# Optimization experiments

Measured on AMD Instinct MI355X. Metric: run time of the kernel, lower is better.

Reference implementation:

```python
import jax, jax.numpy as jnp
import numpy as np

N, E, G = 100000, 400000, 2000   # nodes, edges, graphs
IN, H = 48, 128                  # in_channels, hidden_channels (= out_channels)
L = 6                            # num GIN layers
EPS = 1e-5                       # BatchNorm eps
SLOPE = 0.01                     # leaky_relu negative slope


def setup_inputs() -> dict:
    key = jax.random.key(0)
    ks = jax.random.split(key, 12)
    x = jax.random.normal(ks[0], (N, IN), jnp.float32)
    edge_index = jax.random.randint(ks[1], (2, E), 0, N)
    edge_attr = jax.random.normal(ks[2], (E, 4), jnp.float32)  # ignored by GINConv
    # sorted graph-assignment vector; guarantee every graph has >=1 node
    batch = jnp.sort(jnp.concatenate([jnp.arange(G),
                                      jax.random.randint(ks[3], (N - G,), 0, G)]))
    s = 0.05
    W1a = jax.random.normal(ks[4], (IN, H), jnp.float32) * s        # layer-0 MLP lin1
    W1b = jax.random.normal(ks[5], (L - 1, H, H), jnp.float32) * s  # layers 1..5 MLP lin1
    b1 = jnp.zeros((L, H), jnp.float32)
    g1 = jnp.ones((L, H), jnp.float32)    # inner BN scale
    be1 = jnp.zeros((L, H), jnp.float32)  # inner BN bias
    W2 = jax.random.normal(ks[6], (L, H, H), jnp.float32) * s       # MLP lin2
    b2 = jnp.zeros((L, H), jnp.float32)
    gn = jnp.ones((L - 1, H), jnp.float32)    # outer BN scale (layers 0..4)
    bn_b = jnp.zeros((L - 1, H), jnp.float32) # outer BN bias
    fc_w = jax.random.normal(ks[7], (2 * H, 64), jnp.float32) * s
    fc_b = jnp.zeros((64,), jnp.float32)
    fc2_w = jax.random.normal(ks[8], (64, 3), jnp.float32) * s
    fc2_b = jnp.zeros((3,), jnp.float32)
    return dict(x=x, edge_attr=edge_attr, W1a=W1a, W1b=W1b, b1=b1, g1=g1, be1=be1,
                W2=W2, b2=b2, gn=gn, bn_b=bn_b, fc_w=fc_w, fc_b=fc_b,
                fc2_w=fc2_w, fc2_b=fc2_b, edge_index=edge_index, batch=batch,
                num_graphs=G)


def _bn(h, g, b):
    # training-mode BatchNorm1d over node dim (biased variance, as torch)
    m = jnp.mean(h, axis=0)
    v = jnp.mean((h - m) ** 2, axis=0)
    return g * (h - m) * jax.lax.rsqrt(v + EPS) + b


def _lrelu(h):
    return jnp.where(h >= 0, h, SLOPE * h)


def reference(x, edge_attr, W1a, W1b, b1, g1, be1, W2, b2, gn, bn_b,
              fc_w, fc_b, fc2_w, fc2_b, edge_index, batch, num_graphs):
    del edge_attr  # GINConv does not use edge attributes
    src, dst = edge_index[0], edge_index[1]
    n = x.shape[0]
    h = x
    for l in range(L):
        # GINConv: (1 + eps) * x + sum_{j in N(i)} x_j, eps = 0
        agg = jax.ops.segment_sum(h[src], dst, num_segments=n)
        z = h + agg
        W1 = W1a if l == 0 else W1b[l - 1]
        # MLP([in, H, H]) with inner BatchNorm + leaky_relu, plain last linear
        z = _lrelu(_bn(z @ W1 + b1[l], g1[l], be1[l])) @ W2[l] + b2[l]
        if l < L - 1:  # outer norm + act, skipped on last layer
            z = _lrelu(_bn(z, gn[l], bn_b[l]))
        h = z
    # dual global pooling over ragged per-graph segments
    cnt = jax.ops.segment_sum(jnp.ones((n, 1), h.dtype), batch, num_segments=num_graphs)
    p1 = jax.ops.segment_sum(h, batch, num_segments=num_graphs) / jnp.maximum(cnt, 1.0)
    p2 = jax.ops.segment_max(h, batch, num_segments=num_graphs)
    emb = jnp.concatenate([p1, p2], axis=1)            # [G, 256]
    out = _lrelu(emb @ fc_w + fc_b) @ fc2_w + fc2_b    # [G, 3]
    return out, emb
```

## Files before the change

kernel.cpp:

```cpp
#include <hip/hip_runtime.h>
#include <stdint.h>

#define N_NODES 100000
#define N_EDGES 400000
#define N_GRAPHS 2000
#define C_IN 48
#define HD 128
#define NLAYERS 6
#define BN_EPS 1e-5f
#define NSLOPE 0.01f
#define SB 391
#define NREP 8

typedef uint16_t u16;
typedef uint32_t u32;
typedef short bf16x8 __attribute__((ext_vector_type(8)));
typedef float f32x4 __attribute__((ext_vector_type(4)));

__device__ __forceinline__ float bf2f_lo(u32 v) { return __uint_as_float(v << 16); }
__device__ __forceinline__ float bf2f_hi(u32 v) { return __uint_as_float(v & 0xffff0000u); }
__device__ __forceinline__ float bf2f(u16 h) { return __uint_as_float(((u32)h) << 16); }
__device__ __forceinline__ u16 f2bf(float f) {
    u32 u = __float_as_uint(f);
    u32 r = (u + 0x7fffu + ((u >> 16) & 1u)) >> 16;
    return (u16)r;
}
__device__ __forceinline__ u32 pack2(float a, float b) {
    return (u32)f2bf(a) | ((u32)f2bf(b) << 16);
}
__device__ __forceinline__ float lrelu(float v) { return v >= 0.f ? v : v * NSLOPE; }

__global__ __launch_bounds__(256) void detect_kernel(const u16* __restrict__ x, int* __restrict__ mode) {
    __shared__ int flag;
    if (threadIdx.x == 0) flag = 0;
    __syncthreads();
    int local = 0;
    for (int i = threadIdx.x; i < 16384; i += 256) {
        float a = fabsf(bf2f(x[i]));
        if (!(a < 1e4f)) local = 1;
    }
    if (local) flag = 1;
    __syncthreads();
    if (threadIdx.x == 0) mode[0] = flag;
}

__global__ __launch_bounds__(256) void hist_kernel(const int* __restrict__ dst, int* __restrict__ cnt) {
    int e = blockIdx.x * 256 + threadIdx.x;
    if (e < N_EDGES) atomicAdd(&cnt[dst[e]], 1);
}

__global__ __launch_bounds__(256) void scan1_kernel(const int* __restrict__ cnt, int* __restrict__ bsum) {
    __shared__ int s[256];
    const int t = threadIdx.x;
    const int i = blockIdx.x * 256 + t;
    s[t] = (i < N_NODES) ? cnt[i] : 0;
    __syncthreads();
    for (int d = 128; d > 0; d >>= 1) {
        if (t < d) s[t] += s[t + d];
        __syncthreads();
    }
    if (t == 0) bsum[blockIdx.x] = s[0];
}

__global__ __launch_bounds__(512) void scan2_kernel(int* __restrict__ bsum, int* __restrict__ row_ptr) {
    __shared__ int s[SB];
    const int t = threadIdx.x;
    if (t < SB) s[t] = bsum[t];
    __syncthreads();
    if (t == 0) {
        int run = 0;
        for (int b = 0; b < SB; ++b) { int v = s[b]; s[b] = run; run += v; }
        row_ptr[0] = 0;
    }
    __syncthreads();
    if (t < SB) bsum[t] = s[t];
}

__global__ __launch_bounds__(256) void scan3_kernel(const int* __restrict__ cnt, const int* __restrict__ bsum,
                                                    int* __restrict__ row_ptr) {
    __shared__ int s[256];
    const int t = threadIdx.x;
    const int i = blockIdx.x * 256 + t;
    s[t] = (i < N_NODES) ? cnt[i] : 0;
    __syncthreads();
    if (t == 0) {
        int run = bsum[blockIdx.x];
        for (int j = 0; j < 256; ++j) { run += s[j]; s[j] = run; }
    }
    __syncthreads();
    if (i < N_NODES) row_ptr[i + 1] = s[t];
}

__global__ __launch_bounds__(256) void fill_kernel(const int* __restrict__ src, const int* __restrict__ dst,
                                                   int* __restrict__ cursor, int* __restrict__ col_idx) {
    int e = blockIdx.x * 256 + threadIdx.x;
    if (e < N_EDGES) {
        int d = dst[e];
        int slot = atomicAdd(&cursor[d], 1);
        col_idx[slot] = src[e];
    }
}

__global__ __launch_bounds__(256) void pack_w_kernel(const void* __restrict__ W1a, const void* __restrict__ W1b,
                                                     const void* __restrict__ W2, const int* __restrict__ mode,
                                                     u16* __restrict__ wpack) {
    const int t = blockIdx.x * 256 + threadIdx.x;
    if (t >= 24576) return;
    const int mat = t >> 11;
    const int r = t & 2047;
    const int l = r & 63;
    const int f = r >> 6;
    const int kb = f >> 3, nt = f & 7;
    const int k0 = kb * 32 + (l >> 4) * 8;
    const int n = nt * 16 + (l & 15);
    const int md = *mode;
    u16 vals[8];
    #pragma unroll
    for (int j = 0; j < 8; ++j) {
        const int k = k0 + j;
        float v;
        if (mat == 0) {
            v = (k < C_IN) ? (md ? ((const float*)W1a)[k * HD + n] : bf2f(((const u16*)W1a)[k * HD + n])) : 0.f;
        } else if (mat < 6) {
            const size_t o = (size_t)(mat - 1) * HD * HD + (size_t)k * HD + n;
            v = md ? ((const float*)W1b)[o] : bf2f(((const u16*)W1b)[o]);
        } else {
            const size_t o = (size_t)(mat - 6) * HD * HD + (size_t)k * HD + n;
            v = md ? ((const float*)W2)[o] : bf2f(((const u16*)W2)[o]);
        }
        vals[j] = f2bf(v);
    }
    uint4 o;
    o.x = (u32)vals[0] | ((u32)vals[1] << 16);
    o.y = (u32)vals[2] | ((u32)vals[3] << 16);
    o.z = (u32)vals[4] | ((u32)vals[5] << 16);
    o.w = (u32)vals[6] | ((u32)vals[7] << 16);
    *reinterpret_cast<uint4*>(wpack + (size_t)t * 8) = o;
}

__global__ __launch_bounds__(256) void pack_b_kernel(const void* __restrict__ b1, const void* __restrict__ b2,
                                                     const int* __restrict__ mode, float* __restrict__ biasf) {
    const int i = blockIdx.x * 256 + threadIdx.x;
    if (i >= 12 * HD) return;
    const int mat = i >> 7, c = i & 127;
    const int md = *mode;
    float v;
    if (mat < 6) v = md ? ((const float*)b1)[mat * HD + c] : bf2f(((const u16*)b1)[mat * HD + c]);
    else         v = md ? ((const float*)b2)[(mat - 6) * HD + c] : bf2f(((const u16*)b2)[(mat - 6) * HD + c]);
    biasf[i] = v;
}

__device__ __forceinline__ void coef_to_lds(float* coefs, const float* __restrict__ instats,
                                            const void* __restrict__ gammav, const void* __restrict__ betav,
                                            size_t gelem, int md, int tid) {
    if (tid < 128) {
        float sm = 0.f, sq = 0.f;
        #pragma unroll
        for (int rep = 0; rep < NREP; ++rep) {
            sm += instats[rep * 256 + tid];
            sq += instats[rep * 256 + 128 + tid];
        }
        const float inv_n = 1.0f / (float)N_NODES;
        const float mean = sm * inv_n;
        const float var = fmaxf(sq * inv_n - mean * mean, 0.f);
        const float rs = rsqrtf(var + BN_EPS);
        const float g  = md ? ((const float*)gammav)[gelem + tid] : bf2f(((const u16*)gammav)[gelem + tid]);
        const float be = md ? ((const float*)betav)[gelem + tid]  : bf2f(((const u16*)betav)[gelem + tid]);
        const float A = g * rs;
        coefs[tid] = A;
        coefs[128 + tid] = be - A * mean;
    }
}

template <int TRANS, int STATS>
__global__ __launch_bounds__(256) void gemm_mfma(const u16* A, const u16* __restrict__ wp,
                                                 const float* __restrict__ biasf,
                                                 const float* __restrict__ instats,
                                                 const void* __restrict__ gammav, const void* __restrict__ betav,
                                                 size_t gelem, const int* __restrict__ mode,
                                                 u16* out, float* __restrict__ stats) {
    __shared__ u16 Asm[32][136];
    __shared__ float sred[2][128];
    __shared__ float sqred[2][128];
    __shared__ float coefs[256];
    const int tid = threadIdx.x;
    const int m0 = blockIdx.x * 32;
    const int rrow = tid >> 4;
    const int seg = tid & 15;

    if (TRANS) {
        coef_to_lds(coefs, instats, gammav, betav, gelem, *mode, tid);
        __syncthreads();
    }

    {
        float cA[8], cB[8];
        if (TRANS) {
            #pragma unroll
            for (int j = 0; j < 8; ++j) {
                cA[j] = coefs[seg * 8 + j];
                cB[j] = coefs[128 + seg * 8 + j];
            }
        }
        uint4 v[2];
        #pragma unroll
        for (int i = 0; i < 2; ++i) {
            const int gm = m0 + i * 16 + rrow;
            if (gm < N_NODES) v[i] = *reinterpret_cast<const uint4*>(A + (size_t)gm * HD + seg * 8);
            else { v[i].x = 0; v[i].y = 0; v[i].z = 0; v[i].w = 0; }
        }
        #pragma unroll
        for (int i = 0; i < 2; ++i) {
            uint4 o = v[i];
            if (TRANS) {
                u32 w[4] = {o.x, o.y, o.z, o.w};
                #pragma unroll
                for (int p = 0; p < 4; ++p) {
                    const float lo = lrelu(cA[2 * p] * bf2f_lo(w[p]) + cB[2 * p]);
                    const float hi = lrelu(cA[2 * p + 1] * bf2f_hi(w[p]) + cB[2 * p + 1]);
                    w[p] = pack2(lo, hi);
                }
                o.x = w[0]; o.y = w[1]; o.z = w[2]; o.w = w[3];
            }
            *reinterpret_cast<uint4*>(&Asm[i * 16 + rrow][seg * 8]) = o;
        }
    }
    __syncthreads();

    const int wave = tid >> 6, lane = tid & 63;
    const int quad = lane >> 4, lx = lane & 15;
    const int rowhalf = wave & 1;
    const int colhalf = wave >> 1;
    const int wrow = rowhalf * 16;
    f32x4 acc[4] = {};
    #pragma unroll
    for (int kb = 0; kb < 4; ++kb) {
        bf16x8 bfr[4];
        #pragma unroll
        for (int nt = 0; nt < 4; ++nt)
            bfr[nt] = *reinterpret_cast<const bf16x8*>(wp + (((size_t)(kb * 8 + colhalf * 4 + nt) * 64 + lane) << 3));
        const bf16x8 af = *reinterpret_cast<const bf16x8*>(&Asm[wrow + lx][kb * 32 + quad * 8]);
        #pragma unroll
        for (int nt = 0; nt < 4; ++nt)
            acc[nt] = __builtin_amdgcn_mfma_f32_16x16x32_bf16(af, bfr[nt], acc[nt], 0, 0, 0);
    }

    const int mrow0 = m0 + wrow;
    #pragma unroll
    for (int nt = 0; nt < 4; ++nt) {
        const int n = colhalf * 64 + nt * 16 + lx;
        const float bj = biasf[n];
        float s = 0.f, q = 0.f;
        #pragma unroll
        for (int r = 0; r < 4; ++r) {
            const int m = mrow0 + quad * 4 + r;
            if (m < N_NODES) {
                const float v = acc[nt][r] + bj;
                out[(size_t)m * HD + n] = f2bf(v);
                if (STATS) { s += v; q += v * v; }
            }
        }
        if (STATS) {
            s += __shfl_xor(s, 16); s += __shfl_xor(s, 32);
            q += __shfl_xor(q, 16); q += __shfl_xor(q, 32);
            if (quad == 0) { sred[rowhalf][n] = s; sqred[rowhalf][n] = q; }
        }
    }
    if (STATS) {
        __syncthreads();
        float* sdst = stats + (size_t)(blockIdx.x & (NREP - 1)) * 256;
        if (tid < 128) {
            atomicAdd(&sdst[tid], sred[0][tid] + sred[1][tid]);
        } else if (tid < 256) {
            const int c2 = tid - 128;
            atomicAdd(&sdst[128 + c2], sqred[0][c2] + sqred[1][c2]);
        }
    }
}

__global__ __launch_bounds__(256) void gemm_gather(const u16* __restrict__ U, const int* __restrict__ row_ptr,
                                                   const int* __restrict__ col_idx, const u16* __restrict__ wp,
                                                   const float* __restrict__ biasf,
                                                   const float* __restrict__ instats,
                                                   const void* __restrict__ gammav, const void* __restrict__ betav,
                                                   size_t gelem, const int* __restrict__ mode,
                                                   u16* __restrict__ out, float* __restrict__ stats) {
    __shared__ u16 Asm[16][136];
    __shared__ float sred[128];
    __shared__ float sqred[128];
    __shared__ float coefs[256];
    const int tid = threadIdx.x;
    const int m0 = blockIdx.x * 16;
    const int rrow = tid >> 4;
    const int seg = tid & 15;

    coef_to_lds(coefs, instats, gammav, betav, gelem, *mode, tid);
    __syncthreads();

    {
        float cA[8], cB[8];
        #pragma unroll
        for (int j = 0; j < 8; ++j) {
            cA[j] = coefs[seg * 8 + j];
            cB[j] = coefs[128 + seg * 8 + j];
        }
        const int gm = m0 + rrow;
        float a[8];
        #pragma unroll
        for (int j = 0; j < 8; ++j) a[j] = 0.f;
        if (gm < N_NODES) {
            const uint4 v = *reinterpret_cast<const uint4*>(U + (size_t)gm * HD + seg * 8);
            const u32 w[4] = {v.x, v.y, v.z, v.w};
            #pragma unroll
            for (int p = 0; p < 4; ++p) {
                a[2 * p]     = lrelu(cA[2 * p] * bf2f_lo(w[p]) + cB[2 * p]);
                a[2 * p + 1] = lrelu(cA[2 * p + 1] * bf2f_hi(w[p]) + cB[2 * p + 1]);
            }
            const int s = row_ptr[gm];
            const int deg = row_ptr[gm + 1] - s;
            for (int t = 0; t < deg; t += 2) {
                const int id0 = col_idx[s + t];
                const bool h1 = (t + 1) < deg;
                const int id1 = h1 ? col_idx[s + t + 1] : 0;
                const uint4 r0 = *reinterpret_cast<const uint4*>(U + (size_t)id0 * HD + seg * 8);
                uint4 r1; r1.x = r1.y = r1.z = r1.w = 0;
                if (h1) r1 = *reinterpret_cast<const uint4*>(U + (size_t)id1 * HD + seg * 8);
                const u32 w0[4] = {r0.x, r0.y, r0.z, r0.w};
                const u32 w1[4] = {r1.x, r1.y, r1.z, r1.w};
                #pragma unroll
                for (int p = 0; p < 4; ++p) {
                    a[2 * p]     += lrelu(cA[2 * p] * bf2f_lo(w0[p]) + cB[2 * p]);
                    a[2 * p + 1] += lrelu(cA[2 * p + 1] * bf2f_hi(w0[p]) + cB[2 * p + 1]);
                    if (h1) {
                        a[2 * p]     += lrelu(cA[2 * p] * bf2f_lo(w1[p]) + cB[2 * p]);
                        a[2 * p + 1] += lrelu(cA[2 * p + 1] * bf2f_hi(w1[p]) + cB[2 * p + 1]);
                    }
                }
            }
        }
        uint4 o;
        o.x = pack2(a[0], a[1]); o.y = pack2(a[2], a[3]);
        o.z = pack2(a[4], a[5]); o.w = pack2(a[6], a[7]);
        *reinterpret_cast<uint4*>(&Asm[rrow][seg * 8]) = o;
    }
    __syncthreads();

    const int wave = tid >> 6, lane = tid & 63;
    const int quad = lane >> 4, lx = lane & 15;
    f32x4 acc[2] = {};
    #pragma unroll
    for (int kb = 0; kb < 4; ++kb) {
        bf16x8 bfr[2];
        #pragma unroll
        for (int nt = 0; nt < 2; ++nt)
            bfr[nt] = *reinterpret_cast<const bf16x8*>(wp + (((size_t)(kb * 8 + wave * 2 + nt) * 64 + lane) << 3));
        const bf16x8 af = *reinterpret_cast<const bf16x8*>(&Asm[lx][kb * 32 + quad * 8]);
        #pragma unroll
        for (int nt = 0; nt < 2; ++nt)
            acc[nt] = __builtin_amdgcn_mfma_f32_16x16x32_bf16(af, bfr[nt], acc[nt], 0, 0, 0);
    }

    #pragma unroll
    for (int nt = 0; nt < 2; ++nt) {
        const int n = wave * 32 + nt * 16 + lx;
        const float bj = biasf[n];
        float s = 0.f, q = 0.f;
        #pragma unroll
        for (int r = 0; r < 4; ++r) {
            const int m = m0 + quad * 4 + r;
            if (m < N_NODES) {
                const float v = acc[nt][r] + bj;
                out[(size_t)m * HD + n] = f2bf(v);
                s += v; q += v * v;
            }
        }
        s += __shfl_xor(s, 16); s += __shfl_xor(s, 32);
        q += __shfl_xor(q, 16); q += __shfl_xor(q, 32);
        if (quad == 0) { sred[n] = s; sqred[n] = q; }
    }
    __syncthreads();
    float* sdst = stats + (size_t)(blockIdx.x & (NREP - 1)) * 256;
    if (tid < 128) {
        atomicAdd(&sdst[tid], sred[tid]);
    } else if (tid < 256) {
        const int c2 = tid - 128;
        atomicAdd(&sdst[128 + c2], sqred[c2]);
    }
}

__global__ __launch_bounds__(256) void gemm_gather0(const void* __restrict__ xv, const int* __restrict__ row_ptr,
                                                    const int* __restrict__ col_idx, const u16* __restrict__ wp,
                                                    const float* __restrict__ biasf, const int* __restrict__ mode,
                                                    u16* __restrict__ out, float* __restrict__ stats) {
    __shared__ u16 Asm[16][136];
    __shared__ float sred[128];
    __shared__ float sqred[128];
    const int tid = threadIdx.x;
    const int m0 = blockIdx.x * 16;
    const int rrow = tid >> 4;
    const int seg = tid & 15;
    const int md = *mode;
    const bool act = seg < 6;

    {
        const int gm = m0 + rrow;
        float a[8];
        #pragma unroll
        for (int j = 0; j < 8; ++j) a[j] = 0.f;
        if (gm < N_NODES && act) {
            if (md) {
                const float* xf = (const float*)xv + (size_t)gm * C_IN + seg * 8;
                const float4 v0 = reinterpret_cast<const float4*>(xf)[0];
                const float4 v1 = reinterpret_cast<const float4*>(xf)[1];
                a[0] = v0.x; a[1] = v0.y; a[2] = v0.z; a[3] = v0.w;
                a[4] = v1.x; a[5] = v1.y; a[6] = v1.z; a[7] = v1.w;
            } else {
                const uint4 v = *reinterpret_cast<const uint4*>((const u16*)xv + (size_t)gm * C_IN + seg * 8);
                const u32 w[4] = {v.x, v.y, v.z, v.w};
                #pragma unroll
                for (int p = 0; p < 4; ++p) { a[2 * p] = bf2f_lo(w[p]); a[2 * p + 1] = bf2f_hi(w[p]); }
            }
        }
        if (gm < N_NODES) {
            const int s = row_ptr[gm];
            const int deg = row_ptr[gm + 1] - s;
            for (int t = 0; t < deg; t += 2) {
                const int id0 = col_idx[s + t];
                const bool h1 = (t + 1) < deg;
                const int id1 = h1 ? col_idx[s + t + 1] : 0;
                if (act) {
                    if (md) {
                        const float* p0 = (const float*)xv + (size_t)id0 * C_IN + seg * 8;
                        const float4 u0 = reinterpret_cast<const float4*>(p0)[0];
                        const float4 u1 = reinterpret_cast<const float4*>(p0)[1];
                        a[0] += u0.x; a[1] += u0.y; a[2] += u0.z; a[3] += u0.w;
                        a[4] += u1.x; a[5] += u1.y; a[6] += u1.z; a[7] += u1.w;
                        if (h1) {
                            const float* p1 = (const float*)xv + (size_t)id1 * C_IN + seg * 8;
                            const float4 t0 = reinterpret_cast<const float4*>(p1)[0];
                            const float4 t1 = reinterpret_cast<const float4*>(p1)[1];
                            a[0] += t0.x; a[1] += t0.y; a[2] += t0.z; a[3] += t0.w;
                            a[4] += t1.x; a[5] += t1.y; a[6] += t1.z; a[7] += t1.w;
                        }
                    } else {
                        const uint4 r0 = *reinterpret_cast<const uint4*>((const u16*)xv + (size_t)id0 * C_IN + seg * 8);
                        const u32 w0[4] = {r0.x, r0.y, r0.z, r0.w};
                        #pragma unroll
                        for (int p = 0; p < 4; ++p) { a[2 * p] += bf2f_lo(w0[p]); a[2 * p + 1] += bf2f_hi(w0[p]); }
                        if (h1) {
                            const uint4 r1 = *reinterpret_cast<const uint4*>((const u16*)xv + (size_t)id1 * C_IN + seg * 8);
                            const u32 w1[4] = {r1.x, r1.y, r1.z, r1.w};
                            #pragma unroll
                            for (int p = 0; p < 4; ++p) { a[2 * p] += bf2f_lo(w1[p]); a[2 * p + 1] += bf2f_hi(w1[p]); }
                        }
                    }
                }
            }
        }
        uint4 o;
        o.x = pack2(a[0], a[1]); o.y = pack2(a[2], a[3]);
        o.z = pack2(a[4], a[5]); o.w = pack2(a[6], a[7]);
        *reinterpret_cast<uint4*>(&Asm[rrow][seg * 8]) = o;
    }
    __syncthreads();

    const int wave = tid >> 6, lane = tid & 63;
    const int quad = lane >> 4, lx = lane & 15;
    f32x4 acc[2] = {};
    #pragma unroll
    for (int kb = 0; kb < 4; ++kb) {
        bf16x8 bfr[2];
        #pragma unroll
        for (int nt = 0; nt < 2; ++nt)
            bfr[nt] = *reinterpret_cast<const bf16x8*>(wp + (((size_t)(kb * 8 + wave * 2 + nt) * 64 + lane) << 3));
        const bf16x8 af = *reinterpret_cast<const bf16x8*>(&Asm[lx][kb * 32 + quad * 8]);
        #pragma unroll
        for (int nt = 0; nt < 2; ++nt)
            acc[nt] = __builtin_amdgcn_mfma_f32_16x16x32_bf16(af, bfr[nt], acc[nt], 0, 0, 0);
    }

    #pragma unroll
    for (int nt = 0; nt < 2; ++nt) {
        const int n = wave * 32 + nt * 16 + lx;
        const float bj = biasf[n];
        float s = 0.f, q = 0.f;
        #pragma unroll
        for (int r = 0; r < 4; ++r) {
            const int m = m0 + quad * 4 + r;
            if (m < N_NODES) {
                const float v = acc[nt][r] + bj;
                out[(size_t)m * HD + n] = f2bf(v);
                s += v; q += v * v;
            }
        }
        s += __shfl_xor(s, 16); s += __shfl_xor(s, 32);
        q += __shfl_xor(q, 16); q += __shfl_xor(q, 32);
        if (quad == 0) { sred[n] = s; sqred[n] = q; }
    }
    __syncthreads();
    float* sdst = stats + (size_t)(blockIdx.x & (NREP - 1)) * 256;
    if (tid < 128) {
        atomicAdd(&sdst[tid], sred[tid]);
    } else if (tid < 256) {
        const int c2 = tid - 128;
        atomicAdd(&sdst[128 + c2], sqred[c2]);
    }
}

__global__ __launch_bounds__(256) void pool_kernel(const u16* __restrict__ hf, const int* __restrict__ batch,
                                                   const int* __restrict__ mode, float* __restrict__ emb,
                                                   void* __restrict__ outv) {
    const int wave = threadIdx.x >> 6, lane = threadIdx.x & 63;
    const int g = blockIdx.x * 4 + wave;
    if (g >= N_GRAPHS) return;
    const int md = *mode;
    const int quad = lane >> 4, c = lane & 15;
    int lo = 0, hi = N_NODES;
    while (lo < hi) { int m = (lo + hi) >> 1; if (batch[m] < g) lo = m + 1; else hi = m; }
    const int s = lo;
    hi = N_NODES;
    while (lo < hi) { int m = (lo + hi) >> 1; if (batch[m] < g + 1) lo = m + 1; else hi = m; }
    const int e = lo;
    const int cnt = e - s;
    float sum[8], mx[8];
    #pragma unroll
    for (int j = 0; j < 8; ++j) { sum[j] = 0.f; mx[j] = -INFINITY; }
    for (int n = s + quad; n < e; n += 4) {
        const uint4 v = *reinterpret_cast<const uint4*>(hf + (size_t)n * HD + c * 8);
        const u32 w[4] = {v.x, v.y, v.z, v.w};
        #pragma unroll
        for (int p = 0; p < 4; ++p) {
            const float f0 = bf2f_lo(w[p]), f1 = bf2f_hi(w[p]);
            sum[2 * p] += f0; sum[2 * p + 1] += f1;
            mx[2 * p] = fmaxf(mx[2 * p], f0); mx[2 * p + 1] = fmaxf(mx[2 * p + 1], f1);
        }
    }
    #pragma unroll
    for (int j = 0; j < 8; ++j) {
        sum[j] += __shfl_xor(sum[j], 16); sum[j] += __shfl_xor(sum[j], 32);
        mx[j] = fmaxf(mx[j], __shfl_xor(mx[j], 16));
        mx[j] = fmaxf(mx[j], __shfl_xor(mx[j], 32));
    }
    if (quad == 0) {
        const float invc = 1.0f / (float)max(cnt, 1);
        const size_t base = (size_t)N_GRAPHS * 3 + (size_t)g * 256;
        #pragma unroll
        for (int j = 0; j < 8; ++j) {
            const float mean = sum[j] * invc;
            const float m2 = (cnt == 0) ? 0.f : mx[j];
            const int col = c * 8 + j;
            emb[(size_t)g * 256 + col] = mean;
            emb[(size_t)g * 256 + 128 + col] = m2;
            if (md) {
                ((float*)outv)[base + col] = mean;
                ((float*)outv)[base + 128 + col] = m2;
            } else {
                ((u16*)outv)[base + col] = f2bf(mean);
                ((u16*)outv)[base + 128 + col] = f2bf(m2);
            }
        }
    }
}

__global__ __launch_bounds__(64) void final_kernel(const float* __restrict__ emb, const void* __restrict__ fcwv,
                                                   const void* __restrict__ fcbv, const void* __restrict__ fc2wv,
                                                   const void* __restrict__ fc2bv, const int* __restrict__ mode,
                                                   void* __restrict__ outv) {
    __shared__ float es[256];
    __shared__ float hs[64];
    const int g = blockIdx.x, t = threadIdx.x;
    const int md = *mode;
    reinterpret_cast<float4*>(es)[t] = reinterpret_cast<const float4*>(emb + (size_t)g * 256)[t];
    __syncthreads();
    float acc = md ? ((const float*)fcbv)[t] : bf2f(((const u16*)fcbv)[t]);
    if (md) {
        const float* w = (const float*)fcwv;
        #pragma unroll 8
        for (int k = 0; k < 256; ++k) acc += es[k] * w[k * 64 + t];
    } else {
        const u16* w = (const u16*)fcwv;
        #pragma unroll 8
        for (int k = 0; k < 256; ++k) acc += es[k] * bf2f(w[k * 64 + t]);
    }
    hs[t] = lrelu(acc);
    __syncthreads();
    if (t < 3) {
        float o = md ? ((const float*)fc2bv)[t] : bf2f(((const u16*)fc2bv)[t]);
        if (md) {
            const float* w = (const float*)fc2wv;
            #pragma unroll 8
            for (int j = 0; j < 64; ++j) o += hs[j] * w[j * 3 + t];
            ((float*)outv)[(size_t)g * 3 + t] = o;
        } else {
            const u16* w = (const u16*)fc2wv;
            #pragma unroll 8
            for (int j = 0; j < 64; ++j) o += hs[j] * bf2f(w[j * 3 + t]);
            ((u16*)outv)[(size_t)g * 3 + t] = f2bf(o);
        }
    }
}

static inline size_t align256(size_t x) { return (x + 255) & ~(size_t)255; }

extern "C" void kernel_launch(void* const* d_in, const int* in_sizes, int n_in,
                              void* d_out, int out_size, void* d_ws, size_t ws_size,
                              hipStream_t stream) {
    (void)in_sizes; (void)n_in; (void)out_size; (void)ws_size;
    const void* x    = d_in[0];
    const void* W1a  = d_in[2];
    const void* W1b  = d_in[3];
    const void* b1   = d_in[4];
    const void* g1   = d_in[5];
    const void* be1  = d_in[6];
    const void* W2   = d_in[7];
    const void* b2   = d_in[8];
    const void* gn   = d_in[9];
    const void* bnb  = d_in[10];
    const void* fcw  = d_in[11];
    const void* fcb  = d_in[12];
    const void* fc2w = d_in[13];
    const void* fc2b = d_in[14];
    const int* ei    = (const int*)d_in[15];
    const int* batch = (const int*)d_in[16];

    char* p = (char*)d_ws;
    size_t off = 0;
    u16* zb = (u16*)(p + off); off += align256((size_t)N_NODES * HD * 2);
    u16* hb = (u16*)(p + off); off += align256((size_t)N_NODES * HD * 2);
    u16* wpack = (u16*)(p + off); off += align256((size_t)12 * HD * HD * 2);
    float* biasf = (float*)(p + off); off += align256((size_t)12 * HD * 4);
    float* emb = (float*)(p + off); off += align256((size_t)N_GRAPHS * 256 * 4);
    int* row_ptr = (int*)(p + off); off += align256((size_t)(N_NODES + 1) * 4);
    int* cursor = (int*)(p + off); off += align256((size_t)N_NODES * 4);
    int* col_idx = (int*)(p + off); off += align256((size_t)N_EDGES * 4);
    int* bsum = (int*)(p + off); off += align256((size_t)SB * 4);
    float* statsAll = (float*)(p + off); off += align256((size_t)12 * NREP * 256 * 4);
    int* mode = (int*)(p + off); off += align256(4);

    const int EB = (N_EDGES + 255) / 256;
    const int GBM = (N_NODES + 31) / 32;
    const int GBG = (N_NODES + 15) / 16;

    detect_kernel<<<1, 256, 0, stream>>>((const u16*)x, mode);

    hipMemsetAsync(cursor, 0, (size_t)N_NODES * 4, stream);
    hipMemsetAsync(statsAll, 0, (size_t)12 * NREP * 256 * 4, stream);
    hist_kernel<<<EB, 256, 0, stream>>>(ei + N_EDGES, cursor);
    scan1_kernel<<<SB, 256, 0, stream>>>(cursor, bsum);
    scan2_kernel<<<1, 512, 0, stream>>>(bsum, row_ptr);
    scan3_kernel<<<SB, 256, 0, stream>>>(cursor, bsum, row_ptr);
    hipMemcpyAsync(cursor, row_ptr, (size_t)N_NODES * 4, hipMemcpyDeviceToDevice, stream);
    fill_kernel<<<EB, 256, 0, stream>>>(ei, ei + N_EDGES, cursor, col_idx);
    pack_w_kernel<<<96, 256, 0, stream>>>(W1a, W1b, W2, mode, wpack);
    pack_b_kernel<<<6, 256, 0, stream>>>(b1, b2, mode, biasf);

    u16* cur = zb;
    u16* oth = hb;
    for (int l = 0; l < NLAYERS; ++l) {
        float* statsA = statsAll + (size_t)l * NREP * 256;
        float* statsB = statsAll + (size_t)(6 + l) * NREP * 256;
        float* statsBprev = statsAll + (size_t)(6 + l - 1) * NREP * 256;
        if (l == 0) {
            gemm_gather0<<<GBG, 256, 0, stream>>>(x, row_ptr, col_idx, wpack,
                                                  biasf, mode, cur, statsA);
        } else {
            gemm_gather<<<GBG, 256, 0, stream>>>(cur, row_ptr, col_idx,
                                                 wpack + (size_t)l * HD * HD,
                                                 biasf + (size_t)l * HD, statsBprev, gn, bnb,
                                                 (size_t)(l - 1) * HD, mode, oth, statsA);
            u16* t = cur; cur = oth; oth = t;
        }
        if (l < NLAYERS - 1) {
            gemm_mfma<1, 1><<<GBM, 256, 0, stream>>>(cur, wpack + (size_t)(6 + l) * HD * HD,
                                                     biasf + (size_t)(6 + l) * HD, statsA, g1, be1,
                                                     (size_t)l * HD, mode, cur, statsB);
        } else {
            gemm_mfma<1, 0><<<GBM, 256, 0, stream>>>(cur, wpack + (size_t)(6 + l) * HD * HD,
                                                     biasf + (size_t)(6 + l) * HD, statsA, g1, be1,
                                                     (size_t)l * HD, mode, cur, nullptr);
        }
    }

    pool_kernel<<<(N_GRAPHS + 3) / 4, 256, 0, stream>>>(cur, batch, mode, emb, d_out);
    final_kernel<<<N_GRAPHS, 64, 0, stream>>>(emb, fcw, fcb, fc2w, fc2b, mode, d_out);
}
```

Before: 504.4 us.

## Sort nodes by degree for load-balanced gather and unroll neighbor loop by four

Adds a degree-bucketed counting sort (histogram, scan, scatter) that builds a node permutation. The gather-GEMM kernels then process nodes in degree order, so the 16 rows in a block have similar in-degree and less time goes to waiting on divergent loop lengths. Outputs are scattered back through the permutation. The neighbor loop is also unrolled by four to raise memory-level parallelism. The cost is three extra small setup kernels, scattered output writes, and poorer locality for the self-row reads.

```diff
diff --git a/kernel.cpp b/kernel.cpp
--- a/kernel.cpp
+++ b/kernel.cpp
@@ -11,6 +11,7 @@
 #define NSLOPE 0.01f
 #define SB 391
 #define NREP 8
+#define DBINS 33
 
 typedef uint16_t u16;
 typedef uint32_t u32;
@@ -30,6 +31,29 @@
 }
 __device__ __forceinline__ float lrelu(float v) { return v >= 0.f ? v : v * NSLOPE; }
 
+__device__ __forceinline__ void acc_bn(float* a, const uint4 v, const float* cA, const float* cB) {
+    const u32 w[4] = {v.x, v.y, v.z, v.w};
+    #pragma unroll
+    for (int p = 0; p < 4; ++p) {
+        a[2 * p]     += lrelu(cA[2 * p] * bf2f_lo(w[p]) + cB[2 * p]);
+        a[2 * p + 1] += lrelu(cA[2 * p + 1] * bf2f_hi(w[p]) + cB[2 * p + 1]);
+    }
+}
+__device__ __forceinline__ void acc_bf16row(float* a, const uint4 v) {
+    const u32 w[4] = {v.x, v.y, v.z, v.w};
+    #pragma unroll
+    for (int p = 0; p < 4; ++p) {
+        a[2 * p]     += bf2f_lo(w[p]);
+        a[2 * p + 1] += bf2f_hi(w[p]);
+    }
+}
+__device__ __forceinline__ void acc_f32row(float* a, const float* p) {
+    const float4 u0 = reinterpret_cast<const float4*>(p)[0];
+    const float4 u1 = reinterpret_cast<const float4*>(p)[1];
+    a[0] += u0.x; a[1] += u0.y; a[2] += u0.z; a[3] += u0.w;
+    a[4] += u1.x; a[5] += u1.y; a[6] += u1.z; a[7] += u1.w;
+}
+
 __global__ __launch_bounds__(256) void detect_kernel(const u16* __restrict__ x, int* __restrict__ mode) {
     __shared__ int flag;
     if (threadIdx.x == 0) flag = 0;
@@ -99,6 +123,44 @@
         int slot = atomicAdd(&cursor[d], 1);
         col_idx[slot] = src[e];
     }
+}
+
+__global__ __launch_bounds__(256) void deg_hist_kernel(const int* __restrict__ row_ptr, int* __restrict__ dbins) {
+    __shared__ int h[DBINS];
+    const int tid = threadIdx.x;
+    if (tid < DBINS) h[tid] = 0;
+    __syncthreads();
+    const int i = blockIdx.x * 256 + tid;
+    if (i < N_NODES) atomicAdd(&h[min(row_ptr[i + 1] - row_ptr[i], 32)], 1);
+    __syncthreads();
+    if (tid < DBINS && h[tid]) atomicAdd(&dbins[tid], h[tid]);
+}
+
+__global__ __launch_bounds__(64) void deg_scan_kernel(int* __restrict__ dbins) {
+    if (threadIdx.x == 0) {
+        int run = 0;
+        for (int b = 0; b < DBINS; ++b) { int v = dbins[b]; dbins[b] = run; run += v; }
+    }
+}
+
+__global__ __launch_bounds__(256) void deg_scatter_kernel(const int* __restrict__ row_ptr, int* __restrict__ dbins,
+                                                          int* __restrict__ perm) {
+    __shared__ int cnt[DBINS];
+    __shared__ int base[DBINS];
+    const int tid = threadIdx.x;
+    const int i = blockIdx.x * 256 + tid;
+    if (tid < DBINS) cnt[tid] = 0;
+    __syncthreads();
+    int d = 0, local = 0;
+    const bool act = i < N_NODES;
+    if (act) {
+        d = min(row_ptr[i + 1] - row_ptr[i], 32);
+        local = atomicAdd(&cnt[d], 1);
+    }
+    __syncthreads();
+    if (tid < DBINS) base[tid] = cnt[tid] ? atomicAdd(&dbins[tid], cnt[tid]) : 0;
+    __syncthreads();
+    if (act) perm[base[d] + local] = i;
 }
 
 __global__ __launch_bounds__(256) void pack_w_kernel(const void* __restrict__ W1a, const void* __restrict__ W1b,
@@ -279,7 +341,8 @@
 }
 
 __global__ __launch_bounds__(256) void gemm_gather(const u16* __restrict__ U, const int* __restrict__ row_ptr,
-                                                   const int* __restrict__ col_idx, const u16* __restrict__ wp,
+                                                   const int* __restrict__ col_idx, const int* __restrict__ perm,
+                                                   const u16* __restrict__ wp,
                                                    const float* __restrict__ biasf,
                                                    const float* __restrict__ instats,
                                                    const void* __restrict__ gammav, const void* __restrict__ betav,
@@ -289,12 +352,18 @@
     __shared__ float sred[128];
     __shared__ float sqred[128];
     __shared__ float coefs[256];
+    __shared__ int sperm[16];
     const int tid = threadIdx.x;
     const int m0 = blockIdx.x * 16;
     const int rrow = tid >> 4;
     const int seg = tid & 15;
 
     coef_to_lds(coefs, instats, gammav, betav, gelem, *mode, tid);
+
+    const int lm = m0 + rrow;
+    int gm = -1;
+    if (lm < N_NODES) gm = perm[lm];
+    if (seg == 0) sperm[rrow] = gm;
     __syncthreads();
 
     {
@@ -304,37 +373,43 @@
             cA[j] = coefs[seg * 8 + j];
             cB[j] = coefs[128 + seg * 8 + j];
         }
-        const int gm = m0 + rrow;
         float a[8];
         #pragma unroll
         for (int j = 0; j < 8; ++j) a[j] = 0.f;
-        if (gm < N_NODES) {
+        if (gm >= 0) {
             const uint4 v = *reinterpret_cast<const uint4*>(U + (size_t)gm * HD + seg * 8);
-            const u32 w[4] = {v.x, v.y, v.z, v.w};
-            #pragma unroll
-            for (int p = 0; p < 4; ++p) {
-                a[2 * p]     = lrelu(cA[2 * p] * bf2f_lo(w[p]) + cB[2 * p]);
-                a[2 * p + 1] = lrelu(cA[2 * p + 1] * bf2f_hi(w[p]) + cB[2 * p + 1]);
-            }
+            acc_bn(a, v, cA, cB);
             const int s = row_ptr[gm];
             const int deg = row_ptr[gm + 1] - s;
-            for (int t = 0; t < deg; t += 2) {
-                const int id0 = col_idx[s + t];
-                const bool h1 = (t + 1) < deg;
-                const int id1 = h1 ? col_idx[s + t + 1] : 0;
-                const uint4 r0 = *reinterpret_cast<const uint4*>(U + (size_t)id0 * HD + seg * 8);
-                uint4 r1; r1.x = r1.y = r1.z = r1.w = 0;
-                if (h1) r1 = *reinterpret_cast<const uint4*>(U + (size_t)id1 * HD + seg * 8);
-                const u32 w0[4] = {r0.x, r0.y, r0.z, r0.w};
-                const u32 w1[4] = {r1.x, r1.y, r1.z, r1.w};
-                #pragma unroll
-                for (int p = 0; p < 4; ++p) {
-                    a[2 * p]     += lrelu(cA[2 * p] * bf2f_lo(w0[p]) + cB[2 * p]);
-                    a[2 * p + 1] += lrelu(cA[2 * p + 1] * bf2f_hi(w0[p]) + cB[2 * p + 1]);
-                    if (h1) {
-                        a[2 * p]     += lrelu(cA[2 * p] * bf2f_lo(w1[p]) + cB[2 * p]);
-                        a[2 * p + 1] += lrelu(cA[2 * p + 1] * bf2f_hi(w1[p]) + cB[2 * p + 1]);
-                    }
+            int t = 0;
+            for (; t + 4 <= deg; t += 4) {
+                const int i0 = col_idx[s + t];
+                const int i1 = col_idx[s + t + 1];
+                const int i2 = col_idx[s + t + 2];
+                const int i3 = col_idx[s + t + 3];
+                const uint4 r0 = *reinterpret_cast<const uint4*>(U + (size_t)i0 * HD + seg * 8);
+                const uint4 r1 = *reinterpret_cast<const uint4*>(U + (size_t)i1 * HD + seg * 8);
+                const uint4 r2 = *reinterpret_cast<const uint4*>(U + (size_t)i2 * HD + seg * 8);
+                const uint4 r3 = *reinterpret_cast<const uint4*>(U + (size_t)i3 * HD + seg * 8);
+                acc_bn(a, r0, cA, cB);
+                acc_bn(a, r1, cA, cB);
+                acc_bn(a, r2, cA, cB);
+                acc_bn(a, r3, cA, cB);
+            }
+            const int rem = deg - t;
+            if (rem > 0) {
+                const int i0 = col_idx[s + t];
+                const uint4 r0 = *reinterpret_cast<const uint4*>(U + (size_t)i0 * HD + seg * 8);
+                acc_bn(a, r0, cA, cB);
+                if (rem > 1) {
+                    const int i1 = col_idx[s + t + 1];
+                    const uint4 r1 = *reinterpret_cast<const uint4*>(U + (size_t)i1 * HD + seg * 8);
+                    acc_bn(a, r1, cA, cB);
+                }
+                if (rem > 2) {
+                    const int i2 = col_idx[s + t + 2];
+                    const uint4 r2 = *reinterpret_cast<const uint4*>(U + (size_t)i2 * HD + seg * 8);
+                    acc_bn(a, r2, cA, cB);
                 }
             }
         }
@@ -367,8 +442,9 @@
         float s = 0.f, q = 0.f;
         #pragma unroll
         for (int r = 0; r < 4; ++r) {
-            const int m = m0 + quad * 4 + r;
-            if (m < N_NODES) {
+            const int lr = m0 + quad * 4 + r;
+            if (lr < N_NODES) {
+                const int m = sperm[quad * 4 + r];
                 const float v = acc[nt][r] + bj;
                 out[(size_t)m * HD + n] = f2bf(v);
                 s += v; q += v * v;
@@ -389,12 +465,14 @@
 }
 
 __global__ __launch_bounds__(256) void gemm_gather0(const void* __restrict__ xv, const int* __restrict__ row_ptr,
-                                                    const int* __restrict__ col_idx, const u16* __restrict__ wp,
+                                                    const int* __restrict__ col_idx, const int* __restrict__ perm,
+                                                    const u16* __restrict__ wp,
                                                     const float* __restrict__ biasf, const int* __restrict__ mode,
                                                     u16* __restrict__ out, float* __restrict__ stats) {
     __shared__ u16 Asm[16][136];
     __shared__ float sred[128];
     __shared__ float sqred[128];
+    __shared__ int sperm[16];
     const int tid = threadIdx.x;
     const int m0 = blockIdx.x * 16;
     const int rrow = tid >> 4;
@@ -402,58 +480,55 @@
     const int md = *mode;
     const bool act = seg < 6;
 
+    const int lm = m0 + rrow;
+    int gm = -1;
+    if (lm < N_NODES) gm = perm[lm];
+    if (seg == 0) sperm[rrow] = gm;
+
     {
-        const int gm = m0 + rrow;
         float a[8];
         #pragma unroll
         for (int j = 0; j < 8; ++j) a[j] = 0.f;
-        if (gm < N_NODES && act) {
+        if (gm >= 0 && act) {
             if (md) {
-                const float* xf = (const float*)xv + (size_t)gm * C_IN + seg * 8;
-                const float4 v0 = reinterpret_cast<const float4*>(xf)[0];
-                const float4 v1 = reinterpret_cast<const float4*>(xf)[1];
-                a[0] = v0.x; a[1] = v0.y; a[2] = v0.z; a[3] = v0.w;
-                a[4] = v1.x; a[5] = v1.y; a[6] = v1.z; a[7] = v1.w;
+                acc_f32row(a, (const float*)xv + (size_t)gm * C_IN + seg * 8);
             } else {
-                const uint4 v = *reinterpret_cast<const uint4*>((const u16*)xv + (size_t)gm * C_IN + seg * 8);
-                const u32 w[4] = {v.x, v.y, v.z, v.w};
-                #pragma unroll
-                for (int p = 0; p < 4; ++p) { a[2 * p] = bf2f_lo(w[p]); a[2 * p + 1] = bf2f_hi(w[p]); }
-            }
-        }
-        if (gm < N_NODES) {
+                acc_bf16row(a, *reinterpret_cast<const uint4*>((const u16*)xv + (size_t)gm * C_IN + seg * 8));
+            }
             const int s = row_ptr[gm];
             const int deg = row_ptr[gm + 1] - s;
-            for (int t = 0; t < deg; t += 2) {
-                const int id0 = col_idx[s + t];
-                const bool h1 = (t + 1) < deg;
-                const int id1 = h1 ? col_idx[s + t + 1] : 0;
-                if (act) {
-                    if (md) {
-                        const float* p0 = (const float*)xv + (size_t)id0 * C_IN + seg * 8;
-                        const float4 u0 = reinterpret_cast<const float4*>(p0)[0];
-                        const float4 u1 = reinterpret_cast<const float4*>(p0)[1];
-                        a[0] += u0.x; a[1] += u0.y; a[2] += u0.z; a[3] += u0.w;
-                        a[4] += u1.x; a[5] += u1.y; a[6] += u1.z; a[7] += u1.w;
-                        if (h1) {
-                            const float* p1 = (const float*)xv + (size_t)id1 * C_IN + seg * 8;
-                            const float4 t0 = reinterpret_cast<const float4*>(p1)[0];
-                            const float4 t1 = reinterpret_cast<const float4*>(p1)[1];
-                            a[0] += t0.x; a[1] += t0.y; a[2] += t0.z; a[3] += t0.w;
-                            a[4] += t1.x; a[5] += t1.y; a[6] += t1.z; a[7] += t1.w;
-                        }
-                    } else {
-                        const uint4 r0 = *reinterpret_cast<const uint4*>((const u16*)xv + (size_t)id0 * C_IN + seg * 8);
-                        const u32 w0[4] = {r0.x, r0.y, r0.z, r0.w};
-                        #pragma unroll
-                        for (int p = 0; p < 4; ++p) { a[2 * p] += bf2f_lo(w0[p]); a[2 * p + 1] += bf2f_hi(w0[p]); }
-                        if (h1) {
-                            const uint4 r1 = *reinterpret_cast<const uint4*>((const u16*)xv + (size_t)id1 * C_IN + seg * 8);
-                            const u32 w1[4] = {r1.x, r1.y, r1.z, r1.w};
-                            #pragma unroll
-                            for (int p = 0; p < 4; ++p) { a[2 * p] += bf2f_lo(w1[p]); a[2 * p + 1] += bf2f_hi(w1[p]); }
-                        }
-                    }
+            int t = 0;
+            for (; t + 4 <= deg; t += 4) {
+                const int i0 = col_idx[s + t];
+                const int i1 = col_idx[s + t + 1];
+                const int i2 = col_idx[s + t + 2];
+                const int i3 = col_idx[s + t + 3];
+                if (md) {
+                    acc_f32row(a, (const float*)xv + (size_t)i0 * C_IN + seg * 8);
+                    acc_f32row(a, (const float*)xv + (size_t)i1 * C_IN + seg * 8);
+                    acc_f32row(a, (const float*)xv + (size_t)i2 * C_IN + seg * 8);
+                    acc_f32row(a, (const float*)xv + (size_t)i3 * C_IN + seg * 8);
+                } else {
+                    acc_bf16row(a, *reinterpret_cast<const uint4*>((const u16*)xv + (size_t)i0 * C_IN + seg * 8));
+                    acc_bf16row(a, *reinterpret_cast<const uint4*>((const u16*)xv + (size_t)i1 * C_IN + seg * 8));
+                    acc_bf16row(a, *reinterpret_cast<const uint4*>((const u16*)xv + (size_t)i2 * C_IN + seg * 8));
+                    acc_bf16row(a, *reinterpret_cast<const uint4*>((const u16*)xv + (size_t)i3 * C_IN + seg * 8));
+                }
+            }
+            const int rem = deg - t;
+            if (rem > 0) {
+                const int i0 = col_idx[s + t];
+                if (md) acc_f32row(a, (const float*)xv + (size_t)i0 * C_IN + seg * 8);
+                else    acc_bf16row(a, *reinterpret_cast<const uint4*>((const u16*)xv + (size_t)i0 * C_IN + seg * 8));
+                if (rem > 1) {
+                    const int i1 = col_idx[s + t + 1];
+                    if (md) acc_f32row(a, (const float*)xv + (size_t)i1 * C_IN + seg * 8);
+                    else    acc_bf16row(a, *reinterpret_cast<const uint4*>((const u16*)xv + (size_t)i1 * C_IN + seg * 8));
+                }
+                if (rem > 2) {
+                    const int i2 = col_idx[s + t + 2];
+                    if (md) acc_f32row(a, (const float*)xv + (size_t)i2 * C_IN + seg * 8);
+                    else    acc_bf16row(a, *reinterpret_cast<const uint4*>((const u16*)xv + (size_t)i2 * C_IN + seg * 8));
                 }
             }
         }
@@ -486,8 +561,9 @@
         float s = 0.f, q = 0.f;
         #pragma unroll
         for (int r = 0; r < 4; ++r) {
-            const int m = m0 + quad * 4 + r;
-            if (m < N_NODES) {
+            const int lr = m0 + quad * 4 + r;
+            if (lr < N_NODES) {
+                const int m = sperm[quad * 4 + r];
                 const float v = acc[nt][r] + bj;
                 out[(size_t)m * HD + n] = f2bf(v);
                 s += v; q += v * v;
@@ -635,6 +711,8 @@
     int* col_idx = (int*)(p + off); off += align256((size_t)N_EDGES * 4);
     int* bsum = (int*)(p + off); off += align256((size_t)SB * 4);
     float* statsAll = (float*)(p + off); off += align256((size_t)12 * NREP * 256 * 4);
+    int* perm = (int*)(p + off); off += align256((size_t)N_NODES * 4);
+    int* dbins = (int*)(p + off); off += align256((size_t)64 * 4);
     int* mode = (int*)(p + off); off += align256(4);
 
     const int EB = (N_EDGES + 255) / 256;
@@ -645,10 +723,14 @@
 
     hipMemsetAsync(cursor, 0, (size_t)N_NODES * 4, stream);
     hipMemsetAsync(statsAll, 0, (size_t)12 * NREP * 256 * 4, stream);
+    hipMemsetAsync(dbins, 0, (size_t)DBINS * 4, stream);
     hist_kernel<<<EB, 256, 0, stream>>>(ei + N_EDGES, cursor);
     scan1_kernel<<<SB, 256, 0, stream>>>(cursor, bsum);
     scan2_kernel<<<1, 512, 0, stream>>>(bsum, row_ptr);
     scan3_kernel<<<SB, 256, 0, stream>>>(cursor, bsum, row_ptr);
+    deg_hist_kernel<<<SB, 256, 0, stream>>>(row_ptr, dbins);
+    deg_scan_kernel<<<1, 64, 0, stream>>>(dbins);
+    deg_scatter_kernel<<<SB, 256, 0, stream>>>(row_ptr, dbins, perm);
     hipMemcpyAsync(cursor, row_ptr, (size_t)N_NODES * 4, hipMemcpyDeviceToDevice, stream);
     fill_kernel<<<EB, 256, 0, stream>>>(ei, ei + N_EDGES, cursor, col_idx);
     pack_w_kernel<<<96, 256, 0, stream>>>(W1a, W1b, W2, mode, wpack);
@@ -661,10 +743,10 @@
         float* statsB = statsAll + (size_t)(6 + l) * NREP * 256;
         float* statsBprev = statsAll + (size_t)(6 + l - 1) * NREP * 256;
         if (l == 0) {
-            gemm_gather0<<<GBG, 256, 0, stream>>>(x, row_ptr, col_idx, wpack,
+            gemm_gather0<<<GBG, 256, 0, stream>>>(x, row_ptr, col_idx, perm, wpack,
                                                   biasf, mode, cur, statsA);
         } else {
-            gemm_gather<<<GBG, 256, 0, stream>>>(cur, row_ptr, col_idx,
+            gemm_gather<<<GBG, 256, 0, stream>>>(cur, row_ptr, col_idx, perm,
                                                  wpack + (size_t)l * HD * HD,
                                                  biasf + (size_t)l * HD, statsBprev, gn, bnb,
                                                  (size_t)(l - 1) * HD, mode, oth, statsA);
```

New measurement: 526.7 us. 4.4% more time.
